# Optimization experiments

Measured on AMD Instinct MI355X. Metric: run time of the kernel, lower is better.

Reference implementation:

```python
import jax, jax.numpy as jnp
import numpy as np

B, H, N, D, M = 4, 16, 4096, 64, 256
EPS = 1e-6


def setup_inputs() -> dict:
    key = jax.random.key(0)
    kq, kk, kv, kp = jax.random.split(key, 4)
    q = jax.random.normal(kq, (B, H, N, D), dtype=jnp.float32)
    k = jax.random.normal(kk, (B, H, N, D), dtype=jnp.float32)
    v = jax.random.normal(kv, (B, H, N, D), dtype=jnp.float32)
    # Orthogonal gaussian random-feature matrix [M, D], built like the torch module
    rng = np.random.default_rng(0)
    blocks = []
    n_blocks = M // D
    for _ in range(n_blocks):
        g = rng.standard_normal((D, D))
        qmat, _ = np.linalg.qr(g)
        blocks.append(qmat.T)
    rem = M - n_blocks * D
    if rem > 0:
        g = rng.standard_normal((D, D))
        qmat, _ = np.linalg.qr(g)
        blocks.append(qmat.T[:rem])
    mat = np.concatenate(blocks, axis=0)
    mult = rng.standard_normal((M,))
    proj_mat = jnp.asarray((mult[:, None] * mat).astype(np.float32))
    return {"q": q, "k": k, "v": v, "proj_mat": proj_mat}


def _feature_map(x, proj_mat):
    # x: [b,h,n,d], proj_mat: [m,d] -> [b,h,n,m]; GELU kernel (erf-based, torch default)
    scores = jnp.einsum('bhnd,md->bhnm', x, proj_mat)
    return jax.nn.gelu(scores, approximate=False) + EPS


def reference(q, k, v, proj_mat):
    qp = _feature_map(q, proj_mat)          # [b,h,n,m]
    kp = _feature_map(k, proj_mat)          # [b,h,n,m]
    k_sum = kp.sum(axis=-2)                 # [b,h,m]
    d_inv = 1.0 / jnp.einsum('bhnm,bhm->bhn', qp, k_sum)   # [b,h,n]
    contexts = jnp.einsum('bhnm,bhne->bhme', kp, v)         # [b,h,m,e]
    out = jnp.einsum('bhme,bhnm,bhn->bhne', contexts, qp, d_inv)  # [b,h,n,e]
    return out
```

## Files before the change

### kernel.cpp

```cpp
#include <hip/hip_runtime.h>
#include <cstdint>

#define BH    64
#define NSEQ  4096
#define DH    64
#define MF    256
#define EPS   1e-6f

typedef float f32;
typedef __attribute__((ext_vector_type(4))) float f32x4;

#define CTX_FLOATS (BH * MF * 64)
#define WS_FLOATS  (CTX_FLOATS + BH * MF)

__device__ __forceinline__ float gelu_eps(float s) {
    float x  = s * 0.70710678118654752f;
    float ax = fabsf(x);
    float t  = __builtin_amdgcn_rcpf(fmaf(0.3275911f, ax, 1.0f));
    float p  = t * fmaf(t, fmaf(t, fmaf(t, fmaf(t, 1.061405429f, -1.453152027f),
                                        1.421413741f), -0.284496736f), 0.254829592f);
    float e  = __expf(-(ax * ax));
    float er = copysignf(fmaf(-p, e, 1.0f), x);
    return fmaf(0.5f * s, er, fmaf(0.5f, s, EPS));
}

__global__ void zero_ws_kernel(f32x4* __restrict__ p) {
    p[blockIdx.x * 256 + threadIdx.x] = (f32x4){0.f, 0.f, 0.f, 0.f};
}

__device__ __forceinline__ void stage_P(const f32* __restrict__ Pg_, int f, f32x4* sP4) {
    const f32x4* Pg = (const f32x4*)(Pg_ + (size_t)f * 64 * DH);
    f32* base = (f32*)sP4;
    #pragma unroll
    for (int p = 0; p < 2; ++p) {
        int m2 = threadIdx.x + p * 512;
        int feat = m2 >> 4, dq = m2 & 15;
        f32x4 val = Pg[m2];
        #pragma unroll
        for (int jj = 0; jj < 4; ++jj) {
            int d = dq * 4 + jj;
            base[d * 64 + (((feat >> 2) ^ (d & 15)) << 2) + (feat & 3)] = val[jj];
        }
    }
}

__global__ __launch_bounds__(512, 4) void kside_kernel(
    const f32* __restrict__ Kg_, const f32* __restrict__ Vg_,
    const f32* __restrict__ Pg_, f32* __restrict__ ctx_ws,
    f32* __restrict__ ksum_ws)
{
    __shared__ f32x4 sP4[64 * 16];
    __shared__ f32x4 kp4[128 * 16];

    const int tid = threadIdx.x;
    const int bh  = blockIdx.x >> 4;
    const int f   = (blockIdx.x >> 2) & 3;
    const int rg  = blockIdx.x & 3;
    const size_t rowbase0 = (size_t)bh * NSEQ + rg * 1024;

    const int srg = tid >> 4, sfg = tid & 15;
    const int h   = tid >> 8;
    const int t8  = tid & 255;
    const int cfq = t8 & 15, ceg = t8 >> 4;

    stage_P(Pg_, f, sP4);
    __syncthreads();

    f32x4 ctxacc[4];
    f32x4 ksacc = (f32x4){0.f, 0.f, 0.f, 0.f};
    #pragma unroll
    for (int fi = 0; fi < 4; ++fi) ctxacc[fi] = (f32x4){0.f, 0.f, 0.f, 0.f};

    for (int t = 0; t < 8; ++t) {
        const f32* Kg = Kg_ + (rowbase0 + t * 128) * DH;

        f32x4 s[4];
        #pragma unroll
        for (int r = 0; r < 4; ++r) s[r] = (f32x4){0.f, 0.f, 0.f, 0.f};
        #pragma unroll 4
        for (int kb = 0; kb < 16; ++kb) {
            f32x4 a[4];
            #pragma unroll
            for (int r = 0; r < 4; ++r)
                a[r] = *(const f32x4*)(Kg + (size_t)(srg * 4 + r) * DH + kb * 4);
            #pragma unroll
            for (int kk = 0; kk < 4; ++kk) {
                int d = kb * 4 + kk;
                f32x4 b = sP4[d * 16 + (sfg ^ (d & 15))];
                #pragma unroll
                for (int r = 0; r < 4; ++r) s[r] += a[r][kk] * b;
            }
        }
        #pragma unroll
        for (int r = 0; r < 4; ++r) {
            int row = srg * 4 + r;
            f32x4 g;
            #pragma unroll
            for (int i = 0; i < 4; ++i) g[i] = gelu_eps(s[r][i]);
            kp4[row * 16 + (sfg ^ (row & 15))] = g;
        }
        __syncthreads();

        const f32* Vg = Vg_ + (rowbase0 + t * 128 + h * 64) * DH;
        #pragma unroll 2
        for (int rb = 0; rb < 16; ++rb) {
            f32x4 a4[4], b4[4];
            #pragma unroll
            for (int rr = 0; rr < 4; ++rr) {
                int row = h * 64 + rb * 4 + rr;
                a4[rr] = kp4[row * 16 + (cfq ^ (row & 15))];
                b4[rr] = *(const f32x4*)(Vg + (size_t)(rb * 4 + rr) * DH + ceg * 4);
            }
            #pragma unroll
            for (int rr = 0; rr < 4; ++rr)
                #pragma unroll
                for (int fi = 0; fi < 4; ++fi)
                    ctxacc[fi] += a4[rr][fi] * b4[rr];
            if (ceg == 0) {
                #pragma unroll
                for (int rr = 0; rr < 4; ++rr) ksacc += a4[rr];
            }
        }
        __syncthreads();
    }

    f32* cb = ctx_ws + ((size_t)bh * MF + f * 64 + cfq * 4) * 64 + ceg * 4;
    #pragma unroll
    for (int fi = 0; fi < 4; ++fi)
        #pragma unroll
        for (int ei = 0; ei < 4; ++ei)
            atomicAdd(cb + (size_t)fi * 64 + ei, ctxacc[fi][ei]);
    if (ceg == 0) {
        f32* kb_ = ksum_ws + (size_t)bh * MF + f * 64 + cfq * 4;
        #pragma unroll
        for (int fi = 0; fi < 4; ++fi) atomicAdd(kb_ + fi, ksacc[fi]);
    }
}

__global__ __launch_bounds__(512, 4) void qside_kernel(
    const f32* __restrict__ Qg_, const f32* __restrict__ Pg_,
    const f32* __restrict__ ctx_ws, const f32* __restrict__ ksum_ws,
    f32* __restrict__ out)
{
    __shared__ f32x4 qp4[128 * 16];
    __shared__ f32x4 sP4[64 * 16];
    __shared__ f32x4 sks[64];

    const int tid = threadIdx.x;
    const int bh  = blockIdx.x >> 5;
    const int ch  = blockIdx.x & 31;
    const size_t rowbase = (size_t)bh * NSEQ + ch * 128;

    const int srg = tid >> 4, sfg = tid & 15;
    const int org = tid >> 4, oeg = tid & 15;

    if (tid < 64) sks[tid] = ((const f32x4*)(ksum_ws + (size_t)bh * MF))[tid];

    const f32* Qg = Qg_ + rowbase * DH;

    f32x4 num[4];
    float den[4] = {0.f, 0.f, 0.f, 0.f};
    #pragma unroll
    for (int r = 0; r < 4; ++r) num[r] = (f32x4){0.f, 0.f, 0.f, 0.f};

    for (int f = 0; f < 4; ++f) {
        stage_P(Pg_, f, sP4);
        __syncthreads();

        f32x4 s[4];
        #pragma unroll
        for (int r = 0; r < 4; ++r) s[r] = (f32x4){0.f, 0.f, 0.f, 0.f};
        #pragma unroll 4
        for (int kb = 0; kb < 16; ++kb) {
            f32x4 a[4];
            #pragma unroll
            for (int r = 0; r < 4; ++r)
                a[r] = *(const f32x4*)(Qg + (size_t)(srg * 4 + r) * DH + kb * 4);
            #pragma unroll
            for (int kk = 0; kk < 4; ++kk) {
                int d = kb * 4 + kk;
                f32x4 b = sP4[d * 16 + (sfg ^ (d & 15))];
                #pragma unroll
                for (int r = 0; r < 4; ++r) s[r] += a[r][kk] * b;
            }
        }
        #pragma unroll
        for (int r = 0; r < 4; ++r) {
            int row = srg * 4 + r;
            f32x4 g;
            #pragma unroll
            for (int i = 0; i < 4; ++i) g[i] = gelu_eps(s[r][i]);
            qp4[row * 16 + (sfg ^ (row & 15))] = g;
        }
        __syncthreads();

        const f32* Cg = ctx_ws + ((size_t)bh * MF + f * 64) * 64;
        #pragma unroll 2
        for (int kb = 0; kb < 16; ++kb) {
            f32x4 a[4];
            #pragma unroll
            for (int r = 0; r < 4; ++r) {
                int row = org * 4 + r;
                a[r] = qp4[row * 16 + (kb ^ (row & 15))];
            }
            f32x4 ks = sks[f * 16 + kb];
            #pragma unroll
            for (int kk = 0; kk < 4; ++kk) {
                f32x4 b = *(const f32x4*)(Cg + (size_t)(kb * 4 + kk) * 64 + oeg * 4);
                #pragma unroll
                for (int r = 0; r < 4; ++r) num[r] += a[r][kk] * b;
            }
            #pragma unroll
            for (int r = 0; r < 4; ++r)
                den[r] += a[r][0] * ks[0] + a[r][1] * ks[1] + a[r][2] * ks[2] + a[r][3] * ks[3];
        }
    }

    #pragma unroll
    for (int r = 0; r < 4; ++r) {
        int row = org * 4 + r;
        float dinv = 1.0f / den[r];
        *(f32x4*)(out + (rowbase + row) * DH + oeg * 4) = num[r] * dinv;
    }
}

extern "C" void kernel_launch(void* const* d_in, const int* in_sizes, int n_in,
                              void* d_out, int out_size, void* d_ws, size_t ws_size,
                              hipStream_t stream) {
    const f32* q    = (const f32*)d_in[0];
    const f32* k    = (const f32*)d_in[1];
    const f32* v    = (const f32*)d_in[2];
    const f32* proj = (const f32*)d_in[3];
    f32* out     = (f32*)d_out;
    f32* ctx_ws  = (f32*)d_ws;
    f32* ksum_ws = ctx_ws + CTX_FLOATS;

    const int nzero = WS_FLOATS / 4;
    hipLaunchKernelGGL(zero_ws_kernel, dim3(nzero / 256), dim3(256), 0, stream,
                       (f32x4*)d_ws);
    hipLaunchKernelGGL(kside_kernel, dim3(BH * 16), dim3(512), 0, stream,
                       k, v, proj, ctx_ws, ksum_ws);
    hipLaunchKernelGGL(qside_kernel, dim3(BH * 32), dim3(512), 0, stream,
                       q, proj, ctx_ws, ksum_ws, out);
}
```

Before: 1.035 ms.

## Enlarge per-thread register tiles, halve block size, stage context in LDS

Both kernels drop from 512 to 256 threads per block, and each thread now computes 8 rows instead of 4 in the projection matmul. In the k-side context accumulation each thread builds an 8x8 feature-by-value tile instead of a 4x4 one. The k-side grid is halved, so each block walks 2048 rows, and the key sum is reduced through LDS rather than a branch on one lane group. The q-side now copies each context chunk into LDS before the output matmul instead of reading it from global memory. The aim is more arithmetic per loaded value and fewer global reads and atomics, at the cost of more registers, lower occupancy and extra barriers.

```diff
diff --git a/kernel.cpp b/kernel.cpp
--- a/kernel.cpp
+++ b/kernel.cpp
@@ -12,6 +12,8 @@
 
 #define CTX_FLOATS (BH * MF * 64)
 #define WS_FLOATS  (CTX_FLOATS + BH * MF)
+#define ZV ((f32x4){0.f, 0.f, 0.f, 0.f})
+#define SW(q, r) ((q) ^ ((r) & 15))
 
 __device__ __forceinline__ float gelu_eps(float s) {
     float x  = s * 0.70710678118654752f;
@@ -25,125 +27,135 @@
 }
 
 __global__ void zero_ws_kernel(f32x4* __restrict__ p) {
-    p[blockIdx.x * 256 + threadIdx.x] = (f32x4){0.f, 0.f, 0.f, 0.f};
-}
-
-__device__ __forceinline__ void stage_P(const f32* __restrict__ Pg_, int f, f32x4* sP4) {
+    p[blockIdx.x * 256 + threadIdx.x] = ZV;
+}
+
+__device__ __forceinline__ void stage_P(const f32* __restrict__ Pg_, int f,
+                                        f32x4* sP, int tid) {
     const f32x4* Pg = (const f32x4*)(Pg_ + (size_t)f * 64 * DH);
-    f32* base = (f32*)sP4;
-    #pragma unroll
-    for (int p = 0; p < 2; ++p) {
-        int m2 = threadIdx.x + p * 512;
+    f32* base = (f32*)sP;
+    #pragma unroll
+    for (int p = 0; p < 4; ++p) {
+        int m2 = tid + p * 256;
         int feat = m2 >> 4, dq = m2 & 15;
         f32x4 val = Pg[m2];
         #pragma unroll
         for (int jj = 0; jj < 4; ++jj) {
             int d = dq * 4 + jj;
-            base[d * 64 + (((feat >> 2) ^ (d & 15)) << 2) + (feat & 3)] = val[jj];
-        }
-    }
-}
-
-__global__ __launch_bounds__(512, 4) void kside_kernel(
+            base[d * 64 + (SW(feat >> 2, d) << 2) + (feat & 3)] = val[jj];
+        }
+    }
+}
+
+__global__ __launch_bounds__(256, 2) void kside_kernel(
     const f32* __restrict__ Kg_, const f32* __restrict__ Vg_,
     const f32* __restrict__ Pg_, f32* __restrict__ ctx_ws,
     f32* __restrict__ ksum_ws)
 {
-    __shared__ f32x4 sP4[64 * 16];
-    __shared__ f32x4 kp4[128 * 16];
+    __shared__ f32x4 sP[64 * 16];
+    __shared__ f32x4 kp[128 * 16];
 
     const int tid = threadIdx.x;
-    const int bh  = blockIdx.x >> 4;
-    const int f   = (blockIdx.x >> 2) & 3;
-    const int rg  = blockIdx.x & 3;
-    const size_t rowbase0 = (size_t)bh * NSEQ + rg * 1024;
+    const int b   = blockIdx.x;
+    const int f   = b & 3;
+    const int rg2 = (b >> 2) & 1;
+    const int bh  = b >> 3;
+    const size_t rowbase = (size_t)bh * NSEQ + rg2 * 2048;
 
     const int srg = tid >> 4, sfg = tid & 15;
-    const int h   = tid >> 8;
-    const int t8  = tid & 255;
-    const int cfq = t8 & 15, ceg = t8 >> 4;
-
-    stage_P(Pg_, f, sP4);
+    const int g = tid >> 6, t6 = tid & 63;
+    const int cfg = t6 >> 3, ceg = t6 & 7;
+
+    stage_P(Pg_, f, sP, tid);
     __syncthreads();
 
-    f32x4 ctxacc[4];
-    f32x4 ksacc = (f32x4){0.f, 0.f, 0.f, 0.f};
-    #pragma unroll
-    for (int fi = 0; fi < 4; ++fi) ctxacc[fi] = (f32x4){0.f, 0.f, 0.f, 0.f};
-
-    for (int t = 0; t < 8; ++t) {
-        const f32* Kg = Kg_ + (rowbase0 + t * 128) * DH;
-
-        f32x4 s[4];
-        #pragma unroll
-        for (int r = 0; r < 4; ++r) s[r] = (f32x4){0.f, 0.f, 0.f, 0.f};
+    f32x4 ctxacc[8][2];
+    f32x4 ksp = ZV;
+    #pragma unroll
+    for (int fi = 0; fi < 8; ++fi) { ctxacc[fi][0] = ZV; ctxacc[fi][1] = ZV; }
+
+    for (int t = 0; t < 16; ++t) {
+        const f32* Kg = Kg_ + (rowbase + t * 128) * DH;
+
+        f32x4 s[8];
+        #pragma unroll
+        for (int j = 0; j < 8; ++j) s[j] = ZV;
         #pragma unroll 4
         for (int kb = 0; kb < 16; ++kb) {
-            f32x4 a[4];
-            #pragma unroll
-            for (int r = 0; r < 4; ++r)
-                a[r] = *(const f32x4*)(Kg + (size_t)(srg * 4 + r) * DH + kb * 4);
+            f32x4 a[8];
+            #pragma unroll
+            for (int j = 0; j < 8; ++j)
+                a[j] = *(const f32x4*)(Kg + (size_t)(srg * 8 + j) * DH + kb * 4);
             #pragma unroll
             for (int kk = 0; kk < 4; ++kk) {
                 int d = kb * 4 + kk;
-                f32x4 b = sP4[d * 16 + (sfg ^ (d & 15))];
+                f32x4 bq = sP[d * 16 + SW(sfg, d)];
                 #pragma unroll
-                for (int r = 0; r < 4; ++r) s[r] += a[r][kk] * b;
-            }
-        }
-        #pragma unroll
-        for (int r = 0; r < 4; ++r) {
-            int row = srg * 4 + r;
-            f32x4 g;
-            #pragma unroll
-            for (int i = 0; i < 4; ++i) g[i] = gelu_eps(s[r][i]);
-            kp4[row * 16 + (sfg ^ (row & 15))] = g;
-        }
-        __syncthreads();
-
-        const f32* Vg = Vg_ + (rowbase0 + t * 128 + h * 64) * DH;
-        #pragma unroll 2
-        for (int rb = 0; rb < 16; ++rb) {
-            f32x4 a4[4], b4[4];
-            #pragma unroll
-            for (int rr = 0; rr < 4; ++rr) {
-                int row = h * 64 + rb * 4 + rr;
-                a4[rr] = kp4[row * 16 + (cfq ^ (row & 15))];
-                b4[rr] = *(const f32x4*)(Vg + (size_t)(rb * 4 + rr) * DH + ceg * 4);
-            }
-            #pragma unroll
-            for (int rr = 0; rr < 4; ++rr)
-                #pragma unroll
-                for (int fi = 0; fi < 4; ++fi)
-                    ctxacc[fi] += a4[rr][fi] * b4[rr];
-            if (ceg == 0) {
-                #pragma unroll
-                for (int rr = 0; rr < 4; ++rr) ksacc += a4[rr];
-            }
-        }
-        __syncthreads();
-    }
-
-    f32* cb = ctx_ws + ((size_t)bh * MF + f * 64 + cfq * 4) * 64 + ceg * 4;
-    #pragma unroll
-    for (int fi = 0; fi < 4; ++fi)
-        #pragma unroll
-        for (int ei = 0; ei < 4; ++ei)
-            atomicAdd(cb + (size_t)fi * 64 + ei, ctxacc[fi][ei]);
-    if (ceg == 0) {
-        f32* kb_ = ksum_ws + (size_t)bh * MF + f * 64 + cfq * 4;
-        #pragma unroll
-        for (int fi = 0; fi < 4; ++fi) atomicAdd(kb_ + fi, ksacc[fi]);
-    }
-}
-
-__global__ __launch_bounds__(512, 4) void qside_kernel(
+                for (int j = 0; j < 8; ++j) s[j] += a[j][kk] * bq;
+            }
+        }
+        f32x4 gq[8];
+        #pragma unroll
+        for (int j = 0; j < 8; ++j) {
+            #pragma unroll
+            for (int i = 0; i < 4; ++i) gq[j][i] = gelu_eps(s[j][i]);
+            ksp += gq[j];
+        }
+        __syncthreads();
+        #pragma unroll
+        for (int j = 0; j < 8; ++j) {
+            int row = srg * 8 + j;
+            kp[row * 16 + SW(sfg, row)] = gq[j];
+        }
+        __syncthreads();
+
+        const f32* Vg = Vg_ + (rowbase + t * 128 + g * 32) * DH;
+        #pragma unroll 4
+        for (int k = 0; k < 32; ++k) {
+            int row = g * 32 + k;
+            f32x4 a0 = kp[row * 16 + SW(2 * cfg,     row)];
+            f32x4 a1 = kp[row * 16 + SW(2 * cfg + 1, row)];
+            f32x4 b0 = *(const f32x4*)(Vg + (size_t)k * DH + ceg * 8);
+            f32x4 b1 = *(const f32x4*)(Vg + (size_t)k * DH + ceg * 8 + 4);
+            #pragma unroll
+            for (int fi = 0; fi < 4; ++fi) {
+                ctxacc[fi][0]     += a0[fi] * b0;
+                ctxacc[fi][1]     += a0[fi] * b1;
+                ctxacc[4 + fi][0] += a1[fi] * b0;
+                ctxacc[4 + fi][1] += a1[fi] * b1;
+            }
+        }
+    }
+
+    __syncthreads();
+    ((f32x4*)kp)[sfg * 16 + srg] = ksp;
+    __syncthreads();
+    if (tid < 16) {
+        f32x4 sum = ZV;
+        #pragma unroll
+        for (int r = 0; r < 16; ++r) sum += ((f32x4*)kp)[tid * 16 + r];
+        f32* kb_ = ksum_ws + (size_t)bh * MF + f * 64 + tid * 4;
+        #pragma unroll
+        for (int i = 0; i < 4; ++i) atomicAdd(kb_ + i, sum[i]);
+    }
+
+    f32* cb = ctx_ws + ((size_t)bh * MF + f * 64 + cfg * 8) * 64 + ceg * 8;
+    #pragma unroll
+    for (int fi = 0; fi < 8; ++fi)
+        #pragma unroll
+        for (int h = 0; h < 2; ++h)
+            #pragma unroll
+            for (int ei = 0; ei < 4; ++ei)
+                atomicAdd(cb + (size_t)fi * 64 + h * 4 + ei, ctxacc[fi][h][ei]);
+}
+
+__global__ __launch_bounds__(256, 2) void qside_kernel(
     const f32* __restrict__ Qg_, const f32* __restrict__ Pg_,
     const f32* __restrict__ ctx_ws, const f32* __restrict__ ksum_ws,
     f32* __restrict__ out)
 {
-    __shared__ f32x4 qp4[128 * 16];
-    __shared__ f32x4 sP4[64 * 16];
+    __shared__ f32x4 qp[128 * 16];
+    __shared__ f32x4 sU[64 * 16];
     __shared__ f32x4 sks[64];
 
     const int tid = threadIdx.x;
@@ -151,76 +163,87 @@
     const int ch  = blockIdx.x & 31;
     const size_t rowbase = (size_t)bh * NSEQ + ch * 128;
 
-    const int srg = tid >> 4, sfg = tid & 15;
-    const int org = tid >> 4, oeg = tid & 15;
+    const int rg = tid >> 4, cg = tid & 15;
 
     if (tid < 64) sks[tid] = ((const f32x4*)(ksum_ws + (size_t)bh * MF))[tid];
 
     const f32* Qg = Qg_ + rowbase * DH;
 
-    f32x4 num[4];
-    float den[4] = {0.f, 0.f, 0.f, 0.f};
-    #pragma unroll
-    for (int r = 0; r < 4; ++r) num[r] = (f32x4){0.f, 0.f, 0.f, 0.f};
+    f32x4 num[8];
+    float den[8];
+    #pragma unroll
+    for (int j = 0; j < 8; ++j) { num[j] = ZV; den[j] = 0.f; }
 
     for (int f = 0; f < 4; ++f) {
-        stage_P(Pg_, f, sP4);
-        __syncthreads();
-
-        f32x4 s[4];
-        #pragma unroll
-        for (int r = 0; r < 4; ++r) s[r] = (f32x4){0.f, 0.f, 0.f, 0.f};
+        stage_P(Pg_, f, sU, tid);
+        __syncthreads();
+
+        f32x4 s[8];
+        #pragma unroll
+        for (int j = 0; j < 8; ++j) s[j] = ZV;
         #pragma unroll 4
         for (int kb = 0; kb < 16; ++kb) {
-            f32x4 a[4];
-            #pragma unroll
-            for (int r = 0; r < 4; ++r)
-                a[r] = *(const f32x4*)(Qg + (size_t)(srg * 4 + r) * DH + kb * 4);
+            f32x4 a[8];
+            #pragma unroll
+            for (int j = 0; j < 8; ++j)
+                a[j] = *(const f32x4*)(Qg + (size_t)(rg * 8 + j) * DH + kb * 4);
             #pragma unroll
             for (int kk = 0; kk < 4; ++kk) {
                 int d = kb * 4 + kk;
-                f32x4 b = sP4[d * 16 + (sfg ^ (d & 15))];
+                f32x4 bq = sU[d * 16 + SW(cg, d)];
                 #pragma unroll
-                for (int r = 0; r < 4; ++r) s[r] += a[r][kk] * b;
-            }
-        }
-        #pragma unroll
-        for (int r = 0; r < 4; ++r) {
-            int row = srg * 4 + r;
-            f32x4 g;
-            #pragma unroll
-            for (int i = 0; i < 4; ++i) g[i] = gelu_eps(s[r][i]);
-            qp4[row * 16 + (sfg ^ (row & 15))] = g;
-        }
-        __syncthreads();
-
-        const f32* Cg = ctx_ws + ((size_t)bh * MF + f * 64) * 64;
-        #pragma unroll 2
+                for (int j = 0; j < 8; ++j) s[j] += a[j][kk] * bq;
+            }
+        }
+        #pragma unroll
+        for (int j = 0; j < 8; ++j) {
+            int row = rg * 8 + j;
+            f32x4 gq;
+            #pragma unroll
+            for (int i = 0; i < 4; ++i) gq[i] = gelu_eps(s[j][i]);
+            qp[row * 16 + SW(cg, row)] = gq;
+        }
+        __syncthreads();
+
+        {
+            const f32x4* Cg = (const f32x4*)(ctx_ws + ((size_t)bh * MF + f * 64) * 64);
+            #pragma unroll
+            for (int p = 0; p < 4; ++p) {
+                int m2 = tid + p * 256;
+                int k = m2 >> 4, eq = m2 & 15;
+                sU[k * 16 + SW(eq, k)] = Cg[m2];
+            }
+        }
+        __syncthreads();
+
+        #pragma unroll 4
         for (int kb = 0; kb < 16; ++kb) {
-            f32x4 a[4];
-            #pragma unroll
-            for (int r = 0; r < 4; ++r) {
-                int row = org * 4 + r;
-                a[r] = qp4[row * 16 + (kb ^ (row & 15))];
+            f32x4 a[8];
+            #pragma unroll
+            for (int j = 0; j < 8; ++j) {
+                int row = rg * 8 + j;
+                a[j] = qp[row * 16 + SW(kb, row)];
             }
             f32x4 ks = sks[f * 16 + kb];
             #pragma unroll
             for (int kk = 0; kk < 4; ++kk) {
-                f32x4 b = *(const f32x4*)(Cg + (size_t)(kb * 4 + kk) * 64 + oeg * 4);
+                int k = kb * 4 + kk;
+                f32x4 bq = sU[k * 16 + SW(cg, k)];
                 #pragma unroll
-                for (int r = 0; r < 4; ++r) num[r] += a[r][kk] * b;
-            }
-            #pragma unroll
-            for (int r = 0; r < 4; ++r)
-                den[r] += a[r][0] * ks[0] + a[r][1] * ks[1] + a[r][2] * ks[2] + a[r][3] * ks[3];
-        }
-    }
-
-    #pragma unroll
-    for (int r = 0; r < 4; ++r) {
-        int row = org * 4 + r;
-        float dinv = 1.0f / den[r];
-        *(f32x4*)(out + (rowbase + row) * DH + oeg * 4) = num[r] * dinv;
+                for (int j = 0; j < 8; ++j) num[j] += a[j][kk] * bq;
+            }
+            #pragma unroll
+            for (int j = 0; j < 8; ++j)
+                den[j] += a[j][0] * ks[0] + a[j][1] * ks[1]
+                        + a[j][2] * ks[2] + a[j][3] * ks[3];
+        }
+        __syncthreads();
+    }
+
+    #pragma unroll
+    for (int j = 0; j < 8; ++j) {
+        float dinv = 1.0f / den[j];
+        *(f32x4*)(out + (rowbase + rg * 8 + j) * DH + cg * 4) = num[j] * dinv;
     }
 }
 
@@ -235,11 +258,10 @@
     f32* ctx_ws  = (f32*)d_ws;
     f32* ksum_ws = ctx_ws + CTX_FLOATS;
 
-    const int nzero = WS_FLOATS / 4;
-    hipLaunchKernelGGL(zero_ws_kernel, dim3(nzero / 256), dim3(256), 0, stream,
-                       (f32x4*)d_ws);
-    hipLaunchKernelGGL(kside_kernel, dim3(BH * 16), dim3(512), 0, stream,
+    hipLaunchKernelGGL(zero_ws_kernel, dim3(WS_FLOATS / 4 / 256), dim3(256), 0,
+                       stream, (f32x4*)d_ws);
+    hipLaunchKernelGGL(kside_kernel, dim3(BH * 8), dim3(256), 0, stream,
                        k, v, proj, ctx_ws, ksum_ws);
-    hipLaunchKernelGGL(qside_kernel, dim3(BH * 32), dim3(512), 0, stream,
+    hipLaunchKernelGGL(qside_kernel, dim3(BH * 32), dim3(256), 0, stream,
                        q, proj, ctx_ws, ksum_ws, out);
 }
```

Measured after the change: 924.5 us. -10.7%, faster.
